# Kernel tuning notes

Measured on AMD Instinct MI355X. Metric: run time of the kernel, lower is better.

## Reference

```python
import jax, jax.numpy as jnp
import numpy as np
import math

B, W, N = 48, 100, 1000
EMB, H, QKV, LOCAL = 128, 8, 16, 100
L = LOCAL + 1  # depot + local_size neighbors


def pos_enc(length):
    # sinusoidal positional encoding, emb_dim even so no pad needed
    nts = EMB // 2
    inv = jnp.exp(jnp.arange(nts, dtype=jnp.float32) * (-math.log(10000.0) / max(nts - 1, 1)))
    pos = jnp.arange(length, dtype=jnp.float32)
    st = pos[:, None] * inv[None, :]
    return jnp.concatenate([jnp.sin(st), jnp.cos(st)], axis=1)  # [length, EMB]


def setup_inputs() -> dict:
    key = jax.random.key(0)
    ks = jax.random.split(key, 11)
    return {
        "theta": jax.random.uniform(ks[0], (B, W, N), dtype=jnp.float32),
        "dist": jax.random.uniform(ks[1], (B, W, N), dtype=jnp.float32),
        "xy": jax.random.uniform(ks[2], (B, W, N, 2), dtype=jnp.float32),
        "norm_demand": jax.random.uniform(ks[3], (B, W, N), dtype=jnp.float32),
        "ninf_mask": jnp.zeros((B, W, N), jnp.float32),
        "init_w": jax.random.normal(ks[4], (3, EMB), dtype=jnp.float32) * 0.1,
        "init_b": jnp.zeros((EMB,), jnp.float32),
        "cur_token": jax.random.uniform(ks[5], (EMB,), minval=-1.0, maxval=1.0, dtype=jnp.float32),
        "Wq": jax.random.normal(ks[6], (EMB, H * QKV), dtype=jnp.float32) * 0.05,
        "Wk": jax.random.normal(ks[7], (EMB, H * QKV), dtype=jnp.float32) * 0.05,
        "Wv": jax.random.normal(ks[8], (EMB, H * QKV), dtype=jnp.float32) * 0.05,
        "Wc_w": jax.random.normal(ks[9], (H * QKV, EMB), dtype=jnp.float32) * 0.05,
        "Wc_b": jnp.zeros((EMB,), jnp.float32),
    }


def reference(theta, dist, xy, norm_demand, ninf_mask, init_w, init_b, cur_token, Wq, Wk, Wv, Wc_w, Wc_b):
    # depot always masked: dist -= mask => depot distance -> +inf
    mask = ninf_mask.at[:, :, 0].set(-jnp.inf)
    dist_eff = dist - mask  # [B,W,N]

    # k smallest distances among non-depot nodes (topk largest=False)
    neg_vals, idx0 = jax.lax.top_k(-dist_eff[:, :, 1:], LOCAL)
    dvals = -neg_vals
    dvals = jnp.where(jnp.isinf(dvals), 0.0, dvals)
    norm_on = (jnp.max(dvals, axis=-1) != 0.0)[..., None]          # [B,W,1]
    norm_fac = jnp.max(dvals, axis=-1, keepdims=True) + 1e-6       # [B,W,1]

    depot = jnp.zeros((B, W, 1), idx0.dtype)
    idx = jnp.concatenate([depot, idx0 + 1], axis=-1)              # [B,W,L]

    g = lambda a: jnp.take_along_axis(a, idx, axis=-1)
    sd = g(dist_eff)
    sdem = g(norm_demand)
    sm = g(ninf_mask)
    sx = g(xy[..., 0])
    sy = g(xy[..., 1])

    # zero out inf entries (the masked depot slot)
    infm = jnp.isinf(sd)
    sdem = jnp.where(infm, 0.0, sdem)
    sx = jnp.where(infm, 0.0, sx)
    sy = jnp.where(infm, 0.0, sy)

    # per-(b,w) coordinate normalization by max local distance
    sx = jnp.where(norm_on, sx / norm_fac, sx)
    sy = jnp.where(norm_on, sy / norm_fac, sy)

    # euclidean + demand => 3 input features
    sorted_input = jnp.stack([sx, sy, sdem], axis=-1)              # [B,W,L,3]
    init_k = sorted_input @ init_w + init_b + pos_enc(L)[None, None]  # [B,W,L,EMB]

    # cur_token is identical for every (b,w) -> shared query per head
    q = (cur_token @ Wq).reshape(H, QKV)
    k = (init_k @ Wk).reshape(B, W, L, H, QKV)
    v = (init_k @ Wv).reshape(B, W, L, H, QKV)

    score = jnp.einsum('hd,bwlhd->bwhl', q, k) / float(np.sqrt(QKV)) + sm[:, :, None, :]
    attn = jax.nn.softmax(score, axis=-1)
    out = jnp.einsum('bwhl,bwlhd->bwhd', attn, v).reshape(B, W, H * QKV)

    mh = out @ Wc_w + Wc_b                                         # [B,W,EMB]
    score2 = jnp.einsum('bwe,bwle->bwl', mh, init_k) / float(np.sqrt(EMB))

    bi = jnp.arange(B)[:, None, None]
    wi = jnp.arange(W)[None, :, None]
    return jnp.zeros((B, W, N), score2.dtype).at[bi, wi, idx].set(score2)
```

## Files before the change

### kernel.cpp

```cpp
#include <hip/hip_runtime.h>
#include <math.h>

#define Bb   48
#define Ww   100
#define Nn   1000
#define EMB  128
#define Hh   8
#define LL   101
#define LOCALK 100
#define TPB  256

typedef _Float16 half2v __attribute__((ext_vector_type(2)));
typedef _Float16 half8v __attribute__((ext_vector_type(8)));

#define WS_A    0
#define WS_PE   1024
#define WS_AC   13952
#define WS_WVI  13984
#define WS_PEA  14496
#define WS_PEH  15304
#define WS_PVH  21768
#define WS_WCT  28424

__device__ __forceinline__ unsigned f2key(float x) {
    unsigned u = __float_as_uint(x);
    return (u & 0x80000000u) ? ~u : (u | 0x80000000u);
}
__device__ __forceinline__ float key2f(unsigned k) {
    unsigned u = (k & 0x80000000u) ? (k & 0x7fffffffu) : ~k;
    return __uint_as_float(u);
}
__device__ __forceinline__ void dot8(float& c0, float& c1, float& c2, float& c3,
                                     half8v p, half8v a) {
    c0 = __builtin_amdgcn_fdot2(__builtin_shufflevector(p, p, 0, 1),
                                __builtin_shufflevector(a, a, 0, 1), c0, false);
    c1 = __builtin_amdgcn_fdot2(__builtin_shufflevector(p, p, 2, 3),
                                __builtin_shufflevector(a, a, 2, 3), c1, false);
    c2 = __builtin_amdgcn_fdot2(__builtin_shufflevector(p, p, 4, 5),
                                __builtin_shufflevector(a, a, 4, 5), c2, false);
    c3 = __builtin_amdgcn_fdot2(__builtin_shufflevector(p, p, 6, 7),
                                __builtin_shufflevector(a, a, 6, 7), c3, false);
}

__global__ void setup1(const float* __restrict__ cur, const float* __restrict__ Wq,
                       const float* __restrict__ Wk, const float* __restrict__ iw,
                       const float* __restrict__ ib, const float* __restrict__ Wv,
                       float* __restrict__ ws) {
    const int t = threadIdx.x, b = blockIdx.x;
    if (b == 0) {
        __shared__ float qs[EMB];
        __shared__ float as_[Hh * EMB];
        if (t < EMB) {
            float acc = 0.f;
            for (int e = 0; e < EMB; ++e) acc += cur[e] * Wq[e * EMB + t];
            qs[t] = acc;
        }
        __syncthreads();
        for (int i = t; i < Hh * EMB; i += TPB) {
            int h = i >> 7, e = i & 127;
            float acc = 0.f;
            for (int d = 0; d < 16; ++d) acc += Wk[e * EMB + h * 16 + d] * qs[h * 16 + d];
            acc *= 0.25f;
            as_[i] = acc; ws[WS_A + i] = acc;
        }
        __syncthreads();
        if (t < 32) {
            int i = t >> 3, h = t & 7;
            const float* src = (i == 0) ? iw : (i == 1) ? iw + EMB : (i == 2) ? iw + 2 * EMB : ib;
            float acc = 0.f;
            for (int e = 0; e < EMB; ++e) acc += src[e] * as_[h * EMB + e];
            ws[WS_AC + t] = acc;
        }
    } else {
        int base = (b - 1) * TPB + t;
        const float kneg = -0.14619587891040738f;
        if (base < LL * EMB) {
            int l = base >> 7, c = base & 127, ic = c & 63;
            float inv = expf((float)ic * kneg);
            float v = (float)l * inv;
            float r = (c < 64) ? sinf(v) : cosf(v);
            ws[WS_PE + base] = r;
            ((_Float16*)(ws + WS_PEH))[base] = (_Float16)r;
        } else if (base < LL * EMB + 512) {
            int j = base - LL * EMB;
            int iv = j >> 7, hd = j & 127;
            const float* src = (iv == 0) ? iw : (iv == 1) ? iw + EMB : (iv == 2) ? iw + 2 * EMB : ib;
            float acc = 0.f;
            for (int e = 0; e < EMB; ++e) acc += src[e] * Wv[e * EMB + hd];
            ws[WS_WVI + j] = acc;
        }
    }
}

__global__ void setup2a(const float* __restrict__ Wv, float* __restrict__ ws) {
    int idx = blockIdx.x * TPB + threadIdx.x;
    if (idx < 128 * 104) {
        int hd = idx / 104, l = idx - hd * 104;
        float acc = 0.f;
        if (l < LL) {
            const float* pr = ws + WS_PE + l * EMB;
            for (int e = 0; e < EMB; ++e) acc += pr[e] * Wv[e * EMB + hd];
        }
        ((_Float16*)(ws + WS_PVH))[idx] = (_Float16)acc;
    } else if (idx < 128 * 104 + Hh * LL) {
        int j = idx - 128 * 104;
        int h = j / LL, l = j - h * LL;
        const float* pr = ws + WS_PE + l * EMB;
        const float* ar = ws + WS_A + h * EMB;
        float acc = 0.f;
        for (int e = 0; e < EMB; ++e) acc += pr[e] * ar[e];
        ws[WS_PEA + j] = acc;
    }
}

__global__ void setup2b(const float* __restrict__ Wcw, float* __restrict__ ws) {
    int idx = blockIdx.x * TPB + threadIdx.x;
    if (idx < 128 * 128) {
        int e = idx >> 7, hd = idx & 127;
        ((_Float16*)(ws + WS_WCT))[idx] = (_Float16)Wcw[hd * EMB + e];
    }
}

__global__ __launch_bounds__(TPB, 8) void main_kernel(
    const float* __restrict__ dist,
    const float* __restrict__ xy,
    const float* __restrict__ ndem,
    const float* __restrict__ ninf,
    const float* __restrict__ iw,
    const float* __restrict__ ib,
    const float* __restrict__ Wcb,
    const float* __restrict__ ws,
    float* __restrict__ out) {

    const int bw   = blockIdx.x;
    const int tid  = threadIdx.x;
    const int lane = tid & 63;
    const int wid  = tid >> 6;
    const float* distRow = dist + (size_t)bw * Nn;
    const float* maskRow = ninf + (size_t)bw * Nn;
    float*       outRow  = out  + (size_t)bw * Nn;

    __shared__ __align__(16) char u0[4096];
    int*   hist4 = (int*)u0;
    float* row   = (float*)u0;

    __shared__ unsigned long long list[104];
    __shared__ int   sel[LL];
    __shared__ float feat3[3 * LL];
    __shared__ float smk[LL];
    __shared__ __align__(16) _Float16 attnh[Hh * 104];
    __shared__ __align__(16) _Float16 uhh[EMB];
    __shared__ float mhf[EMB];
    __shared__ __align__(16) _Float16 mhh[EMB];
    __shared__ float cAC[32];
    __shared__ float coef[Hh][3];
    __shared__ float coefM[4];
    __shared__ int   selSh[3];
    __shared__ int   waveSums[4];
    __shared__ float red[2];
    __shared__ unsigned long long pivotSh;
    __shared__ int   cntSh;

    unsigned long long rk[4];
    #pragma unroll
    for (int r = 0; r < 4; ++r) {
        int i = tid + 256 * r;
        unsigned long long kv = ~0ull;
        if (i >= 1 && i < Nn) {
            float de = distRow[i] - maskRow[i];
            kv = ((unsigned long long)f2key(de) << 32) | (unsigned)i;
        }
        rk[r] = kv;
    }
    #pragma unroll
    for (int r = 0; r < 4; ++r) hist4[tid + 256 * r] = 0;
    __syncthreads();

    unsigned long long prefix = 0;
    int shift = 56;
    int remRank = 99;
    int* myhist = hist4 + (wid << 8);
    for (int round = 0; round < 8; ++round) {
        shift = 56 - 8 * round;
        #pragma unroll
        for (int r = 0; r < 4; ++r) {
            unsigned long long kv = rk[r];
            if (round == 0 || (kv >> (shift + 8)) == (prefix >> (shift + 8)))
                atomicAdd(&myhist[(unsigned)((kv >> shift) & 0xffull)], 1);
        }
        __syncthreads();
        int cnt = hist4[tid] + hist4[256 + tid] + hist4[512 + tid] + hist4[768 + tid];
        hist4[tid] = 0; hist4[256 + tid] = 0; hist4[512 + tid] = 0; hist4[768 + tid] = 0;
        int v = cnt;
        #pragma unroll
        for (int o = 1; o < 64; o <<= 1) {
            int t = __shfl_up(v, o, 64);
            if (lane >= o) v += t;
        }
        if (lane == 63) waveSums[wid] = v;
        __syncthreads();
        int wOff = 0;
        if (wid > 0) wOff += waveSums[0];
        if (wid > 1) wOff += waveSums[1];
        if (wid > 2) wOff += waveSums[2];
        int excl = v + wOff - cnt;
        if (cnt > 0 && remRank >= excl && remRank < excl + cnt) {
            selSh[0] = tid; selSh[1] = excl; selSh[2] = cnt;
        }
        __syncthreads();
        prefix |= ((unsigned long long)selSh[0]) << shift;
        remRank -= selSh[1];
        if (selSh[2] == 1) break;
    }
    #pragma unroll
    for (int r = 0; r < 4; ++r)
        if ((rk[r] >> shift) == (prefix >> shift)) pivotSh = rk[r];
    if (tid == 0) cntSh = 0;
    __syncthreads();
    const unsigned long long pivot = pivotSh;

    #pragma unroll
    for (int r = 0; r < 4; ++r) {
        bool p = rk[r] <= pivot;
        unsigned long long m = __ballot(p);
        int c = __popcll(m);
        int base = 0;
        if (lane == 0 && c) base = atomicAdd(&cntSh, c);
        base = __shfl(base, 0, 64);
        if (p) list[base + __popcll(m & ((1ull << lane) - 1ull))] = rk[r];
    }
    __syncthreads();

    if (tid < 128) {
        float dvm = 0.f;
        if (tid < LOCALK) {
            unsigned long long kv = list[tid];
            int rank = 0;
            for (int j = 0; j < LOCALK; ++j) rank += (list[j] < kv) ? 1 : 0;
            float v = key2f((unsigned)(kv >> 32));
            bool infm = isinf(v);
            sel[rank + 1] = (int)(unsigned)(kv & 0xffffffffu) | (infm ? 0x40000000 : 0);
            dvm = infm ? 0.f : v;
        }
        #pragma unroll
        for (int o = 32; o > 0; o >>= 1) dvm = fmaxf(dvm, __shfl_xor(dvm, o, 64));
        if (lane == 0) red[wid] = dvm;
    } else {
        float4 z = make_float4(0.f, 0.f, 0.f, 0.f);
        float4* r4 = (float4*)row;
        for (int i = tid - 128; i < 250; i += 128) r4[i] = z;
    }
    if (tid == 0) sel[0] = 0x40000000;
    __syncthreads();

    const float nmax = fmaxf(red[0], red[1]);
    const bool  norm_on = (nmax != 0.f);
    const float nfac = nmax + 1e-6f;

    if (tid < LL) {
        int s = sel[tid];
        int n = s & 0xffffff;
        bool infm = (s & 0x40000000) != 0;
        float fx = 0.f, fy = 0.f, fd = 0.f;
        if (!infm) {
            size_t base = (size_t)bw * Nn + n;
            fx = xy[2 * base];
            fy = xy[2 * base + 1];
            fd = ndem[base];
        }
        if (norm_on) { fx /= nfac; fy /= nfac; }
        feat3[tid] = fx; feat3[LL + tid] = fy; feat3[2 * LL + tid] = fd;
        smk[tid] = maskRow[n];
    }
    if (tid >= 224) cAC[tid - 224] = ws[WS_AC + tid - 224];
    __syncthreads();

    {
        int g = tid >> 5, ln = tid & 31;
        int l0 = ln, l1 = ln + 32, l2 = ln + 64, l3 = ln + 96;
        bool ok3 = (l3 < LL);
        const float* pea = ws + WS_PEA + g * LL;
        float A0 = cAC[g], A1 = cAC[8 + g], A2 = cAC[16 + g], C = cAC[24 + g];
        float v0 = feat3[l0] * A0 + feat3[LL + l0] * A1 + feat3[2 * LL + l0] * A2 + C + pea[l0] + smk[l0];
        float v1 = feat3[l1] * A0 + feat3[LL + l1] * A1 + feat3[2 * LL + l1] * A2 + C + pea[l1] + smk[l1];
        float v2 = feat3[l2] * A0 + feat3[LL + l2] * A1 + feat3[2 * LL + l2] * A2 + C + pea[l2] + smk[l2];
        float v3 = ok3 ? (feat3[l3] * A0 + feat3[LL + l3] * A1 + feat3[2 * LL + l3] * A2 + C + pea[l3] + smk[l3])
                       : -INFINITY;
        float m = fmaxf(fmaxf(v0, v1), fmaxf(v2, v3));
        #pragma unroll
        for (int o = 16; o > 0; o >>= 1) m = fmaxf(m, __shfl_xor(m, o, 32));
        float e0 = __expf(v0 - m), e1 = __expf(v1 - m), e2 = __expf(v2 - m);
        float e3 = ok3 ? __expf(v3 - m) : 0.f;
        float s = e0 + e1 + e2 + e3;
        #pragma unroll
        for (int o = 16; o > 0; o >>= 1) s += __shfl_xor(s, o, 32);
        float inv = 1.f / s;
        e0 *= inv; e1 *= inv; e2 *= inv; e3 *= inv;
        attnh[g * 104 + l0] = (_Float16)e0;
        attnh[g * 104 + l1] = (_Float16)e1;
        attnh[g * 104 + l2] = (_Float16)e2;
        if (ok3) attnh[g * 104 + l3] = (_Float16)e3;
        else if (l3 < 104) attnh[g * 104 + l3] = (_Float16)0.f;
        #pragma unroll
        for (int f = 0; f < 3; ++f) {
            const float* fr = feat3 + f * LL;
            float cs = e0 * fr[l0] + e1 * fr[l1] + e2 * fr[l2] + (ok3 ? e3 * fr[l3] : 0.f);
            #pragma unroll
            for (int o = 16; o > 0; o >>= 1) cs += __shfl_xor(cs, o, 32);
            if (ln == 0) coef[g][f] = cs;
        }
    }
    __syncthreads();

    if (tid < 128) {
        int hd = tid, h = hd >> 4;
        const half8v* pv = (const half8v*)((const _Float16*)(ws + WS_PVH) + hd * 104);
        const half8v* at = (const half8v*)(attnh + h * 104);
        float c0 = 0.f, c1 = 0.f, c2 = 0.f, c3 = 0.f;
        #pragma unroll
        for (int j = 0; j < 13; ++j) dot8(c0, c1, c2, c3, pv[j], at[j]);
        float u = (c0 + c1) + (c2 + c3)
                + coef[h][0] * ws[WS_WVI + hd]
                + coef[h][1] * ws[WS_WVI + 128 + hd]
                + coef[h][2] * ws[WS_WVI + 256 + hd]
                + ws[WS_WVI + 384 + hd];
        uhh[hd] = (_Float16)u;
    }
    __syncthreads();

    if (tid < 128) {
        int e = tid;
        const half8v* wr = (const half8v*)((const _Float16*)(ws + WS_WCT) + e * 128);
        const half8v* ur = (const half8v*)uhh;
        float c0 = 0.f, c1 = 0.f, c2 = 0.f, c3 = 0.f;
        #pragma unroll
        for (int j = 0; j < 16; ++j) dot8(c0, c1, c2, c3, wr[j], ur[j]);
        float m = Wcb[e] + (c0 + c1) + (c2 + c3);
        mhf[e] = m; mhh[e] = (_Float16)m;
    }
    __syncthreads();

    {
        int g = tid >> 6;
        const float* src = (g == 0) ? iw : (g == 1) ? iw + EMB : (g == 2) ? iw + 2 * EMB : ib;
        float v = mhf[lane] * src[lane] + mhf[lane + 64] * src[lane + 64];
        #pragma unroll
        for (int o = 32; o > 0; o >>= 1) v += __shfl_xor(v, o, 64);
        if (lane == 0) coefM[g] = v;
    }
    __syncthreads();

    if (tid < LL) {
        float base = feat3[tid] * coefM[0] + feat3[LL + tid] * coefM[1]
                   + feat3[2 * LL + tid] * coefM[2] + coefM[3];
        const half8v* pr = (const half8v*)((const _Float16*)(ws + WS_PEH) + tid * 128);
        const half8v* mr = (const half8v*)mhh;
        float c0 = 0.f, c1 = 0.f, c2 = 0.f, c3 = 0.f;
        #pragma unroll
        for (int j = 0; j < 16; ++j) dot8(c0, c1, c2, c3, pr[j], mr[j]);
        row[sel[tid] & 0xffffff] = (base + (c0 + c1) + (c2 + c3)) * 0.08838834764831845f;
    }
    __syncthreads();

    if (tid < 250) {
        ((float4*)outRow)[tid] = ((float4*)row)[tid];
    }
}

extern "C" void kernel_launch(void* const* d_in, const int* in_sizes, int n_in,
                              void* d_out, int out_size, void* d_ws, size_t ws_size,
                              hipStream_t stream) {
    const float* dist  = (const float*)d_in[1];
    const float* xy    = (const float*)d_in[2];
    const float* ndem  = (const float*)d_in[3];
    const float* ninf  = (const float*)d_in[4];
    const float* initw = (const float*)d_in[5];
    const float* initb = (const float*)d_in[6];
    const float* cur   = (const float*)d_in[7];
    const float* Wq    = (const float*)d_in[8];
    const float* Wk    = (const float*)d_in[9];
    const float* Wv    = (const float*)d_in[10];
    const float* Wcw   = (const float*)d_in[11];
    const float* Wcb   = (const float*)d_in[12];
    float* out = (float*)d_out;
    float* ws  = (float*)d_ws;

    hipLaunchKernelGGL(setup1,  dim3(56), dim3(TPB), 0, stream, cur, Wq, Wk, initw, initb, Wv, ws);
    hipLaunchKernelGGL(setup2a, dim3(56), dim3(TPB), 0, stream, Wv, ws);
    hipLaunchKernelGGL(setup2b, dim3(64), dim3(TPB), 0, stream, Wcw, ws);
    hipLaunchKernelGGL(main_kernel, dim3(Bb * Ww), dim3(TPB), 0, stream,
                       dist, xy, ndem, ninf, initw, initb, Wcb, ws, out);
}
```

Before: 104.4 us.

## Map one (b,w) row per wavefront and replace block barriers with wave syncs

Each 256-thread block now handles four (b,w) rows, one per 64-lane wavefront, each with its own shared-memory arena. The radix top-k select, softmax, attention and projection stages are rewritten for a single wave: 16 keys per lane, a wave-local histogram, and ballot/shuffle in place of block-wide __syncthreads. The aim is to remove block barrier and cross-wave reduction overhead and keep all lanes busy. In exchange each lane holds more registers (16 64-bit keys) and the launch-bounds occupancy hint drops from 8 to 6.

```diff
diff --git a/kernel.cpp b/kernel.cpp
--- a/kernel.cpp
+++ b/kernel.cpp
@@ -9,6 +9,7 @@
 #define LL   101
 #define LOCALK 100
 #define TPB  256
+#define PPB  4
 
 typedef _Float16 half2v __attribute__((ext_vector_type(2)));
 typedef _Float16 half8v __attribute__((ext_vector_type(8)));
@@ -21,6 +22,16 @@
 #define WS_PEH  15304
 #define WS_PVH  21768
 #define WS_WCT  28424
+
+#define AR_SIZE 6528
+#define AR_SEL  4096
+#define AR_F3   4512
+#define AR_SMK  5728
+#define AR_MHH  6144
+#define AR_COEF 6400
+#define AR_CM   6496
+
+#define WSYNC() do { __builtin_amdgcn_wave_barrier(); asm volatile("" ::: "memory"); } while (0)
 
 __device__ __forceinline__ unsigned f2key(float x) {
     unsigned u = __float_as_uint(x);
@@ -121,7 +132,7 @@
     }
 }
 
-__global__ __launch_bounds__(TPB, 8) void main_kernel(
+__global__ __launch_bounds__(TPB, 6) void main_kernel(
     const float* __restrict__ dist,
     const float* __restrict__ xy,
     const float* __restrict__ ndem,
@@ -132,39 +143,32 @@
     const float* __restrict__ ws,
     float* __restrict__ out) {
 
-    const int bw   = blockIdx.x;
+    __shared__ __align__(16) char smem[PPB][AR_SIZE];
     const int tid  = threadIdx.x;
+    const int w    = tid >> 6;
     const int lane = tid & 63;
-    const int wid  = tid >> 6;
+    const int bw   = blockIdx.x * PPB + w;
+
+    char* A = smem[w];
+    int*                hist  = (int*)A;
+    unsigned long long* list  = (unsigned long long*)(A + 1024);
+    _Float16*           attnh = (_Float16*)A;
+    _Float16*           uhh   = (_Float16*)(A + 1792);
+    float*              row   = (float*)A;
+    int*                sel   = (int*)(A + AR_SEL);
+    float*              feat3 = (float*)(A + AR_F3);
+    float*              smk   = (float*)(A + AR_SMK);
+    _Float16*           mhh   = (_Float16*)(A + AR_MHH);
+    float*              coef  = (float*)(A + AR_COEF);
+    float*              coefM = (float*)(A + AR_CM);
+
     const float* distRow = dist + (size_t)bw * Nn;
     const float* maskRow = ninf + (size_t)bw * Nn;
-    float*       outRow  = out  + (size_t)bw * Nn;
-
-    __shared__ __align__(16) char u0[4096];
-    int*   hist4 = (int*)u0;
-    float* row   = (float*)u0;
-
-    __shared__ unsigned long long list[104];
-    __shared__ int   sel[LL];
-    __shared__ float feat3[3 * LL];
-    __shared__ float smk[LL];
-    __shared__ __align__(16) _Float16 attnh[Hh * 104];
-    __shared__ __align__(16) _Float16 uhh[EMB];
-    __shared__ float mhf[EMB];
-    __shared__ __align__(16) _Float16 mhh[EMB];
-    __shared__ float cAC[32];
-    __shared__ float coef[Hh][3];
-    __shared__ float coefM[4];
-    __shared__ int   selSh[3];
-    __shared__ int   waveSums[4];
-    __shared__ float red[2];
-    __shared__ unsigned long long pivotSh;
-    __shared__ int   cntSh;
-
-    unsigned long long rk[4];
-    #pragma unroll
-    for (int r = 0; r < 4; ++r) {
-        int i = tid + 256 * r;
+
+    unsigned long long rk[16];
+    #pragma unroll
+    for (int r = 0; r < 16; ++r) {
+        int i = r * 64 + lane;
         unsigned long long kv = ~0ull;
         if (i >= 1 && i < Nn) {
             float de = distRow[i] - maskRow[i];
@@ -172,199 +176,232 @@
         }
         rk[r] = kv;
     }
-    #pragma unroll
-    for (int r = 0; r < 4; ++r) hist4[tid + 256 * r] = 0;
-    __syncthreads();
+    ((int4*)hist)[lane] = make_int4(0, 0, 0, 0);
+    WSYNC();
 
     unsigned long long prefix = 0;
     int shift = 56;
     int remRank = 99;
-    int* myhist = hist4 + (wid << 8);
+    const unsigned long long ltm = (1ull << lane) - 1ull;
     for (int round = 0; round < 8; ++round) {
         shift = 56 - 8 * round;
         #pragma unroll
-        for (int r = 0; r < 4; ++r) {
+        for (int r = 0; r < 16; ++r) {
             unsigned long long kv = rk[r];
-            if (round == 0 || (kv >> (shift + 8)) == (prefix >> (shift + 8)))
-                atomicAdd(&myhist[(unsigned)((kv >> shift) & 0xffull)], 1);
-        }
-        __syncthreads();
-        int cnt = hist4[tid] + hist4[256 + tid] + hist4[512 + tid] + hist4[768 + tid];
-        hist4[tid] = 0; hist4[256 + tid] = 0; hist4[512 + tid] = 0; hist4[768 + tid] = 0;
-        int v = cnt;
-        #pragma unroll
-        for (int o = 1; o < 64; o <<= 1) {
-            int t = __shfl_up(v, o, 64);
-            if (lane >= o) v += t;
-        }
-        if (lane == 63) waveSums[wid] = v;
-        __syncthreads();
-        int wOff = 0;
-        if (wid > 0) wOff += waveSums[0];
-        if (wid > 1) wOff += waveSums[1];
-        if (wid > 2) wOff += waveSums[2];
-        int excl = v + wOff - cnt;
-        if (cnt > 0 && remRank >= excl && remRank < excl + cnt) {
-            selSh[0] = tid; selSh[1] = excl; selSh[2] = cnt;
-        }
-        __syncthreads();
-        prefix |= ((unsigned long long)selSh[0]) << shift;
-        remRank -= selSh[1];
-        if (selSh[2] == 1) break;
-    }
-    #pragma unroll
-    for (int r = 0; r < 4; ++r)
-        if ((rk[r] >> shift) == (prefix >> shift)) pivotSh = rk[r];
-    if (tid == 0) cntSh = 0;
-    __syncthreads();
-    const unsigned long long pivot = pivotSh;
-
-    #pragma unroll
-    for (int r = 0; r < 4; ++r) {
+            bool in = (kv != ~0ull) &&
+                      (round == 0 || (kv >> (shift + 8)) == (prefix >> (shift + 8)));
+            if (in) atomicAdd(&hist[(unsigned)((kv >> shift) & 0xffull)], 1);
+        }
+        WSYNC();
+        int4 hv = ((int4*)hist)[lane];
+        ((int4*)hist)[lane] = make_int4(0, 0, 0, 0);
+        int s = hv.x + hv.y + hv.z + hv.w;
+        int incl = s;
+        #pragma unroll
+        for (int o = 1; o < 64; o <<= 1) { int t = __shfl_up(incl, o, 64); if (lane >= o) incl += t; }
+        int e0 = incl - s;
+        int e1 = e0 + hv.x, e2 = e1 + hv.y, e3 = e2 + hv.z;
+        int bc = -1, ec = 0, cc = 0;
+        if (hv.x > 0 && remRank >= e0 && remRank < e1)        { bc = 4*lane+0; ec = e0; cc = hv.x; }
+        if (hv.y > 0 && remRank >= e1 && remRank < e2)        { bc = 4*lane+1; ec = e1; cc = hv.y; }
+        if (hv.z > 0 && remRank >= e2 && remRank < e3)        { bc = 4*lane+2; ec = e2; cc = hv.z; }
+        if (hv.w > 0 && remRank >= e3 && remRank < e3+hv.w)   { bc = 4*lane+3; ec = e3; cc = hv.w; }
+        unsigned long long fm = __ballot(bc >= 0);
+        int srcl = __ffsll((unsigned long long)fm) - 1;
+        bc = __shfl(bc, srcl, 64); ec = __shfl(ec, srcl, 64); cc = __shfl(cc, srcl, 64);
+        prefix |= ((unsigned long long)(unsigned)bc) << shift;
+        remRank -= ec;
+        if (cc == 1) break;
+    }
+
+    unsigned long long pk = 0; bool pf = false;
+    #pragma unroll
+    for (int r = 0; r < 16; ++r)
+        if ((rk[r] >> shift) == (prefix >> shift)) { pk = rk[r]; pf = true; }
+    {
+        unsigned long long fm = __ballot(pf);
+        int srcl = __ffsll((unsigned long long)fm) - 1;
+        pk = __shfl(pk, srcl, 64);
+    }
+    const unsigned long long pivot = pk;
+
+    int cnt_run = 0;
+    #pragma unroll
+    for (int r = 0; r < 16; ++r) {
         bool p = rk[r] <= pivot;
         unsigned long long m = __ballot(p);
-        int c = __popcll(m);
-        int base = 0;
-        if (lane == 0 && c) base = atomicAdd(&cntSh, c);
-        base = __shfl(base, 0, 64);
-        if (p) list[base + __popcll(m & ((1ull << lane) - 1ull))] = rk[r];
-    }
-    __syncthreads();
-
-    if (tid < 128) {
-        float dvm = 0.f;
-        if (tid < LOCALK) {
-            unsigned long long kv = list[tid];
-            int rank = 0;
-            for (int j = 0; j < LOCALK; ++j) rank += (list[j] < kv) ? 1 : 0;
-            float v = key2f((unsigned)(kv >> 32));
-            bool infm = isinf(v);
-            sel[rank + 1] = (int)(unsigned)(kv & 0xffffffffu) | (infm ? 0x40000000 : 0);
-            dvm = infm ? 0.f : v;
-        }
-        #pragma unroll
-        for (int o = 32; o > 0; o >>= 1) dvm = fmaxf(dvm, __shfl_xor(dvm, o, 64));
-        if (lane == 0) red[wid] = dvm;
-    } else {
-        float4 z = make_float4(0.f, 0.f, 0.f, 0.f);
-        float4* r4 = (float4*)row;
-        for (int i = tid - 128; i < 250; i += 128) r4[i] = z;
-    }
-    if (tid == 0) sel[0] = 0x40000000;
-    __syncthreads();
-
-    const float nmax = fmaxf(red[0], red[1]);
+        if (p) list[cnt_run + (int)__popcll(m & ltm)] = rk[r];
+        cnt_run += (int)__popcll(m);
+    }
+    WSYNC();
+
+    unsigned long long kv0 = list[lane];
+    const bool has1 = lane < (LOCALK - 64);
+    unsigned long long kv1 = has1 ? list[lane + 64] : ~0ull;
+    int r0 = 0, r1 = 0;
+    #pragma unroll 4
+    for (int j = 0; j < LOCALK; ++j) {
+        unsigned long long lv = list[j];
+        r0 += (lv < kv0);
+        r1 += (lv < kv1);
+    }
+    float v0 = key2f((unsigned)(kv0 >> 32));
+    bool i0 = isinf(v0);
+    sel[r0 + 1] = (int)(kv0 & 0xffffffu) | (i0 ? 0x40000000 : 0);
+    float dvm = i0 ? 0.f : v0;
+    if (has1) {
+        float v1 = key2f((unsigned)(kv1 >> 32));
+        bool i1 = isinf(v1);
+        sel[r1 + 1] = (int)(kv1 & 0xffffffu) | (i1 ? 0x40000000 : 0);
+        dvm = fmaxf(dvm, i1 ? 0.f : v1);
+    }
+    #pragma unroll
+    for (int o = 32; o > 0; o >>= 1) dvm = fmaxf(dvm, __shfl_xor(dvm, o, 64));
+    if (lane == 0) sel[0] = 0x40000000;
+    const float nmax = dvm;
     const bool  norm_on = (nmax != 0.f);
     const float nfac = nmax + 1e-6f;
-
-    if (tid < LL) {
-        int s = sel[tid];
+    WSYNC();
+
+    auto gather1 = [&](int t) {
+        int s = sel[t];
         int n = s & 0xffffff;
         bool infm = (s & 0x40000000) != 0;
         float fx = 0.f, fy = 0.f, fd = 0.f;
         if (!infm) {
             size_t base = (size_t)bw * Nn + n;
-            fx = xy[2 * base];
-            fy = xy[2 * base + 1];
-            fd = ndem[base];
+            fx = xy[2 * base]; fy = xy[2 * base + 1]; fd = ndem[base];
         }
         if (norm_on) { fx /= nfac; fy /= nfac; }
-        feat3[tid] = fx; feat3[LL + tid] = fy; feat3[2 * LL + tid] = fd;
-        smk[tid] = maskRow[n];
-    }
-    if (tid >= 224) cAC[tid - 224] = ws[WS_AC + tid - 224];
-    __syncthreads();
-
+        feat3[t] = fx; feat3[LL + t] = fy; feat3[2 * LL + t] = fd;
+        smk[t] = maskRow[n];
+    };
+    gather1(lane);
+    if (lane < LL - 64) gather1(lane + 64);
+    WSYNC();
+
+    const int h = lane >> 3, ln8 = lane & 7;
     {
-        int g = tid >> 5, ln = tid & 31;
-        int l0 = ln, l1 = ln + 32, l2 = ln + 64, l3 = ln + 96;
-        bool ok3 = (l3 < LL);
-        const float* pea = ws + WS_PEA + g * LL;
-        float A0 = cAC[g], A1 = cAC[8 + g], A2 = cAC[16 + g], C = cAC[24 + g];
-        float v0 = feat3[l0] * A0 + feat3[LL + l0] * A1 + feat3[2 * LL + l0] * A2 + C + pea[l0] + smk[l0];
-        float v1 = feat3[l1] * A0 + feat3[LL + l1] * A1 + feat3[2 * LL + l1] * A2 + C + pea[l1] + smk[l1];
-        float v2 = feat3[l2] * A0 + feat3[LL + l2] * A1 + feat3[2 * LL + l2] * A2 + C + pea[l2] + smk[l2];
-        float v3 = ok3 ? (feat3[l3] * A0 + feat3[LL + l3] * A1 + feat3[2 * LL + l3] * A2 + C + pea[l3] + smk[l3])
-                       : -INFINITY;
-        float m = fmaxf(fmaxf(v0, v1), fmaxf(v2, v3));
-        #pragma unroll
-        for (int o = 16; o > 0; o >>= 1) m = fmaxf(m, __shfl_xor(m, o, 32));
-        float e0 = __expf(v0 - m), e1 = __expf(v1 - m), e2 = __expf(v2 - m);
-        float e3 = ok3 ? __expf(v3 - m) : 0.f;
-        float s = e0 + e1 + e2 + e3;
-        #pragma unroll
-        for (int o = 16; o > 0; o >>= 1) s += __shfl_xor(s, o, 32);
-        float inv = 1.f / s;
-        e0 *= inv; e1 *= inv; e2 *= inv; e3 *= inv;
-        attnh[g * 104 + l0] = (_Float16)e0;
-        attnh[g * 104 + l1] = (_Float16)e1;
-        attnh[g * 104 + l2] = (_Float16)e2;
-        if (ok3) attnh[g * 104 + l3] = (_Float16)e3;
-        else if (l3 < 104) attnh[g * 104 + l3] = (_Float16)0.f;
-        #pragma unroll
-        for (int f = 0; f < 3; ++f) {
-            const float* fr = feat3 + f * LL;
-            float cs = e0 * fr[l0] + e1 * fr[l1] + e2 * fr[l2] + (ok3 ? e3 * fr[l3] : 0.f);
-            #pragma unroll
-            for (int o = 16; o > 0; o >>= 1) cs += __shfl_xor(cs, o, 32);
-            if (ln == 0) coef[g][f] = cs;
-        }
-    }
-    __syncthreads();
-
-    if (tid < 128) {
-        int hd = tid, h = hd >> 4;
+        const float A0 = ws[WS_AC + h], A1 = ws[WS_AC + 8 + h];
+        const float A2 = ws[WS_AC + 16 + h], Cc = ws[WS_AC + 24 + h];
+        const float* pea = ws + WS_PEA + h * LL;
+        float ev[14];
+        float mx = -INFINITY;
+        #pragma unroll
+        for (int k = 0; k < 14; ++k) {
+            int l = ln8 + 8 * k;
+            float sv = -INFINITY;
+            if (l < LL)
+                sv = feat3[l] * A0 + feat3[LL + l] * A1 + feat3[2 * LL + l] * A2
+                   + Cc + pea[l] + smk[l];
+            ev[k] = sv;
+            mx = fmaxf(mx, sv);
+        }
+        #pragma unroll
+        for (int o = 1; o < 8; o <<= 1) mx = fmaxf(mx, __shfl_xor(mx, o, 64));
+        float sm = 0.f;
+        #pragma unroll
+        for (int k = 0; k < 14; ++k) {
+            int l = ln8 + 8 * k;
+            float e = (l < LL) ? __expf(ev[k] - mx) : 0.f;
+            ev[k] = e; sm += e;
+        }
+        #pragma unroll
+        for (int o = 1; o < 8; o <<= 1) sm += __shfl_xor(sm, o, 64);
+        const float ainv = 1.f / sm;
+        #pragma unroll
+        for (int k = 0; k < 14; ++k) {
+            int l = ln8 + 8 * k;
+            attnh[h * 112 + l] = (_Float16)(ev[k] * ainv);
+        }
+        float c0 = 0.f, c1 = 0.f, c2 = 0.f;
+        #pragma unroll
+        for (int k = 0; k < 13; ++k) {
+            int l = ln8 + 8 * k;
+            if (l < LL) {
+                float at = ev[k] * ainv;
+                c0 += at * feat3[l]; c1 += at * feat3[LL + l]; c2 += at * feat3[2 * LL + l];
+            }
+        }
+        #pragma unroll
+        for (int o = 1; o < 8; o <<= 1) {
+            c0 += __shfl_xor(c0, o, 64); c1 += __shfl_xor(c1, o, 64); c2 += __shfl_xor(c2, o, 64);
+        }
+        if (ln8 == 0) { coef[h * 3 + 0] = c0; coef[h * 3 + 1] = c1; coef[h * 3 + 2] = c2; }
+    }
+    WSYNC();
+
+    #pragma unroll
+    for (int t = 0; t < 2; ++t) {
+        int hd = lane + 64 * t;
+        int hh = hd >> 4;
         const half8v* pv = (const half8v*)((const _Float16*)(ws + WS_PVH) + hd * 104);
-        const half8v* at = (const half8v*)(attnh + h * 104);
-        float c0 = 0.f, c1 = 0.f, c2 = 0.f, c3 = 0.f;
-        #pragma unroll
-        for (int j = 0; j < 13; ++j) dot8(c0, c1, c2, c3, pv[j], at[j]);
-        float u = (c0 + c1) + (c2 + c3)
-                + coef[h][0] * ws[WS_WVI + hd]
-                + coef[h][1] * ws[WS_WVI + 128 + hd]
-                + coef[h][2] * ws[WS_WVI + 256 + hd]
+        const half8v* at = (const half8v*)(attnh + hh * 112);
+        float d0 = 0.f, d1 = 0.f, d2 = 0.f, d3 = 0.f;
+        #pragma unroll
+        for (int j = 0; j < 13; ++j) dot8(d0, d1, d2, d3, pv[j], at[j]);
+        float u = (d0 + d1) + (d2 + d3)
+                + coef[hh * 3 + 0] * ws[WS_WVI + hd]
+                + coef[hh * 3 + 1] * ws[WS_WVI + 128 + hd]
+                + coef[hh * 3 + 2] * ws[WS_WVI + 256 + hd]
                 + ws[WS_WVI + 384 + hd];
         uhh[hd] = (_Float16)u;
     }
-    __syncthreads();
-
-    if (tid < 128) {
-        int e = tid;
+    WSYNC();
+
+    #pragma unroll
+    for (int t = 0; t < 2; ++t) {
+        int e = lane + 64 * t;
         const half8v* wr = (const half8v*)((const _Float16*)(ws + WS_WCT) + e * 128);
         const half8v* ur = (const half8v*)uhh;
-        float c0 = 0.f, c1 = 0.f, c2 = 0.f, c3 = 0.f;
-        #pragma unroll
-        for (int j = 0; j < 16; ++j) dot8(c0, c1, c2, c3, wr[j], ur[j]);
-        float m = Wcb[e] + (c0 + c1) + (c2 + c3);
-        mhf[e] = m; mhh[e] = (_Float16)m;
-    }
-    __syncthreads();
+        float d0 = 0.f, d1 = 0.f, d2 = 0.f, d3 = 0.f;
+        #pragma unroll
+        for (int j = 0; j < 16; ++j) dot8(d0, d1, d2, d3, wr[j], ur[j]);
+        mhh[e] = (_Float16)(Wcb[e] + (d0 + d1) + (d2 + d3));
+    }
+    WSYNC();
 
     {
-        int g = tid >> 6;
+        int g = lane & 3;
         const float* src = (g == 0) ? iw : (g == 1) ? iw + EMB : (g == 2) ? iw + 2 * EMB : ib;
-        float v = mhf[lane] * src[lane] + mhf[lane + 64] * src[lane + 64];
-        #pragma unroll
-        for (int o = 32; o > 0; o >>= 1) v += __shfl_xor(v, o, 64);
-        if (lane == 0) coefM[g] = v;
-    }
-    __syncthreads();
-
-    if (tid < LL) {
-        float base = feat3[tid] * coefM[0] + feat3[LL + tid] * coefM[1]
-                   + feat3[2 * LL + tid] * coefM[2] + coefM[3];
-        const half8v* pr = (const half8v*)((const _Float16*)(ws + WS_PEH) + tid * 128);
+        float v = 0.f;
+        #pragma unroll
+        for (int j = 0; j < 8; ++j) {
+            int e = (lane >> 2) + 16 * j;
+            v += (float)mhh[e] * src[e];
+        }
+        v += __shfl_xor(v, 4, 64); v += __shfl_xor(v, 8, 64);
+        v += __shfl_xor(v, 16, 64); v += __shfl_xor(v, 32, 64);
+        if (lane < 4) coefM[lane] = v;
+    }
+    {
+        float4 z = make_float4(0.f, 0.f, 0.f, 0.f);
+        ((float4*)row)[lane] = z;
+        ((float4*)row)[lane + 64] = z;
+        ((float4*)row)[lane + 128] = z;
+        if (lane < 58) ((float4*)row)[lane + 192] = z;
+    }
+    WSYNC();
+
+    auto score2 = [&](int t) {
+        float base = feat3[t] * coefM[0] + feat3[LL + t] * coefM[1]
+                   + feat3[2 * LL + t] * coefM[2] + coefM[3];
+        const half8v* pr = (const half8v*)((const _Float16*)(ws + WS_PEH) + t * 128);
         const half8v* mr = (const half8v*)mhh;
-        float c0 = 0.f, c1 = 0.f, c2 = 0.f, c3 = 0.f;
-        #pragma unroll
-        for (int j = 0; j < 16; ++j) dot8(c0, c1, c2, c3, pr[j], mr[j]);
-        row[sel[tid] & 0xffffff] = (base + (c0 + c1) + (c2 + c3)) * 0.08838834764831845f;
-    }
-    __syncthreads();
-
-    if (tid < 250) {
-        ((float4*)outRow)[tid] = ((float4*)row)[tid];
-    }
+        float d0 = 0.f, d1 = 0.f, d2 = 0.f, d3 = 0.f;
+        #pragma unroll
+        for (int j = 0; j < 16; ++j) dot8(d0, d1, d2, d3, pr[j], mr[j]);
+        row[sel[t] & 0xffffff] = (base + (d0 + d1) + (d2 + d3)) * 0.08838834764831845f;
+    };
+    score2(lane);
+    if (lane < LL - 64) score2(lane + 64);
+    WSYNC();
+
+    float* outRow = out + (size_t)bw * Nn;
+    ((float4*)outRow)[lane]       = ((float4*)row)[lane];
+    ((float4*)outRow)[lane + 64]  = ((float4*)row)[lane + 64];
+    ((float4*)outRow)[lane + 128] = ((float4*)row)[lane + 128];
+    if (lane < 58) ((float4*)outRow)[lane + 192] = ((float4*)row)[lane + 192];
 }
 
 extern "C" void kernel_launch(void* const* d_in, const int* in_sizes, int n_in,
@@ -388,6 +425,6 @@
     hipLaunchKernelGGL(setup1,  dim3(56), dim3(TPB), 0, stream, cur, Wq, Wk, initw, initb, Wv, ws);
     hipLaunchKernelGGL(setup2a, dim3(56), dim3(TPB), 0, stream, Wv, ws);
     hipLaunchKernelGGL(setup2b, dim3(64), dim3(TPB), 0, stream, Wcw, ws);
-    hipLaunchKernelGGL(main_kernel, dim3(Bb * Ww), dim3(TPB), 0, stream,
+    hipLaunchKernelGGL(main_kernel, dim3(Bb * Ww / PPB), dim3(TPB), 0, stream,
                        dist, xy, ndem, ninf, initw, initb, Wcb, ws, out);
 }
```

Result: faster. 101.9 us (-2.4%).
